# Performance work log

Measured on AMD Instinct MI355X. Metric: run time of the kernel, lower is better.

Reference implementation:

```python
import jax, jax.numpy as jnp
import numpy as np

D_MODEL = 1024
N_HEAD = 16
HEAD_SIZE = D_MODEL // N_HEAD


def setup_inputs() -> dict:
    key = jax.random.key(0)
    ks = jax.random.split(key, 7)
    B, T, E = 2, 2048, D_MODEL
    scale = 0.02
    return {
        "q": jax.random.normal(ks[0], (B, T, E), dtype=jnp.float32),
        "k": jax.random.normal(ks[1], (B, T, E), dtype=jnp.float32),
        "v": jax.random.normal(ks[2], (B, T, E), dtype=jnp.float32),
        "Wq": jax.random.normal(ks[3], (E, E), dtype=jnp.float32) * scale,
        "Wk": jax.random.normal(ks[4], (E, E), dtype=jnp.float32) * scale,
        "Wv": jax.random.normal(ks[5], (E, E), dtype=jnp.float32) * scale,
        "Wo": jax.random.normal(ks[6], (E, E), dtype=jnp.float32) * scale,
    }


def reference(q, k, v, Wq, Wk, Wv, Wo):
    B, T, E = q.shape
    # torch nn.Linear(bias=False): y = x @ W.T
    qh = (q @ Wq.T).reshape(B, T, N_HEAD, HEAD_SIZE).transpose(0, 2, 1, 3)  # [B,H,T,Dh]
    kh = (k @ Wk.T).reshape(B, T, N_HEAD, HEAD_SIZE).transpose(0, 2, 1, 3)
    vh = (v @ Wv.T).reshape(B, T, N_HEAD, HEAD_SIZE).transpose(0, 2, 1, 3)

    scale = 1.0 / jnp.sqrt(jnp.asarray(HEAD_SIZE, dtype=q.dtype))
    wei = jnp.einsum("bhqd,bhkd->bhqk", qh, kh) * scale  # [B,H,T,T]

    # causal mask (tril): positions j > i set to -inf
    causal = jnp.tril(jnp.ones((T, T), dtype=bool))
    wei = jnp.where(causal, wei, jnp.asarray(-jnp.inf, dtype=wei.dtype))

    attn = jax.nn.softmax(wei, axis=-1)
    out = jnp.einsum("bhqk,bhkd->bhqd", attn, vh)  # [B,H,T,Dh]
    out = out.transpose(0, 2, 1, 3).reshape(B, T, E)
    return out @ Wo.T  # dropout p=0.0 -> identity
```

## Files before the change

kernel.cpp:

```cpp
#include <hip/hip_runtime.h>
#include <hip/hip_bf16.h>
#include <cstddef>
#include <cstdint>

#define B_SZ   2
#define T_SEQ  2048
#define E_DIM  1024
#define N_HEAD 16
#define HEAD   64

typedef unsigned short u16;
typedef unsigned int u32;
using frag8 = __attribute__((ext_vector_type(8))) short;
using f32x4 = __attribute__((ext_vector_type(4))) float;

__device__ inline u16 f2bf(float x) {
    __hip_bfloat16 h = __float2bfloat16(x);
    return *reinterpret_cast<u16*>(&h);
}

__device__ inline void gl2lds16(const void* g, void* l) {
    auto gp = reinterpret_cast<const __attribute__((address_space(1))) unsigned int*>(
        reinterpret_cast<uintptr_t>(g));
    auto lp = reinterpret_cast<__attribute__((address_space(3))) unsigned int*>(
        reinterpret_cast<uintptr_t>(l));
    __builtin_amdgcn_global_load_lds(gp, lp, 16, 0, 0);
}

struct CastArgs {
    const float* src[7];
    u16* dst[7];
    int n[7];
    float scale[7];
};

__global__ __launch_bounds__(256) void cast_f32_bf16(CastArgs a) {
    const int t = blockIdx.y;
    const int i0 = (blockIdx.x * 256 + threadIdx.x) * 8;
    if (i0 >= a.n[t]) return;
    const float sc = a.scale[t];
    const float4 f0 = *(const float4*)(a.src[t] + i0);
    const float4 f1 = *(const float4*)(a.src[t] + i0 + 4);
    union { u16 s[8]; uint4 v; } r;
    r.s[0] = f2bf(f0.x * sc); r.s[1] = f2bf(f0.y * sc);
    r.s[2] = f2bf(f0.z * sc); r.s[3] = f2bf(f0.w * sc);
    r.s[4] = f2bf(f1.x * sc); r.s[5] = f2bf(f1.y * sc);
    r.s[6] = f2bf(f1.z * sc); r.s[7] = f2bf(f1.w * sc);
    *(uint4*)(a.dst[t] + i0) = r.v;
}

__device__ inline void gemm_core(const u16* __restrict__ X,
                                 const u16* __restrict__ W,
                                 void* __restrict__ Yv, int mode,
                                 int bm0, int bn0) {
    __shared__ u16 As[2][128 * 64];
    __shared__ u16 Bs[2][128 * 64];

    const int tid = threadIdx.x;
    const int w = tid >> 6;
    const int lane = tid & 63;
    const int ln = lane & 15;
    const int quad = lane >> 4;
    const int wm = (w & 1) * 64;
    const int wn = (w >> 1) * 64;

    const int l8 = lane >> 3;
    const int g = (lane & 7) ^ l8;

    const u16* Ag = X + (size_t)(bm0 + w * 32 + l8) * 1024 + g * 8;
    const u16* Bg = W + (size_t)(bn0 + w * 32 + l8) * 1024 + g * 8;
    const int al = __builtin_amdgcn_readfirstlane(w * 2048);
    const int bl = __builtin_amdgcn_readfirstlane(w * 2048);

    const f32x4 zf = {0.f, 0.f, 0.f, 0.f};
    f32x4 acc[4][4];
#pragma unroll
    for (int mi = 0; mi < 4; ++mi)
#pragma unroll
        for (int nj = 0; nj < 4; ++nj) acc[mi][nj] = zf;

    const int sw = ln & 7;

#pragma unroll
    for (int it = 0; it < 4; ++it) {
        gl2lds16(Ag + (size_t)it * 8 * 1024, &As[0][0] + al + it * 512);
        gl2lds16(Bg + (size_t)it * 8 * 1024, &Bs[0][0] + bl + it * 512);
    }

    for (int k0 = 0; k0 < 1024; k0 += 64) {
        const int buf = (k0 >> 6) & 1;
        __syncthreads();

        if (k0 + 64 < 1024) {
#pragma unroll
            for (int it = 0; it < 4; ++it) {
                gl2lds16(Ag + (size_t)it * 8 * 1024 + k0 + 64,
                         &As[buf ^ 1][0] + al + it * 512);
                gl2lds16(Bg + (size_t)it * 8 * 1024 + k0 + 64,
                         &Bs[buf ^ 1][0] + bl + it * 512);
            }
        }

        frag8 a[4][2], b[4][2];
#pragma unroll
        for (int kc = 0; kc < 2; ++kc) {
            const int slot = ((kc * 4 + quad) ^ sw) * 8;
#pragma unroll
            for (int mi = 0; mi < 4; ++mi)
                a[mi][kc] = *(const frag8*)(&As[buf][0] + (wm + mi * 16 + ln) * 64 + slot);
#pragma unroll
            for (int nj = 0; nj < 4; ++nj)
                b[nj][kc] = *(const frag8*)(&Bs[buf][0] + (wn + nj * 16 + ln) * 64 + slot);
        }
#pragma unroll
        for (int kc = 0; kc < 2; ++kc)
#pragma unroll
            for (int mi = 0; mi < 4; ++mi)
#pragma unroll
                for (int nj = 0; nj < 4; ++nj)
                    acc[mi][nj] = __builtin_amdgcn_mfma_f32_16x16x32_bf16(
                        a[mi][kc], b[nj][kc], acc[mi][nj], 0, 0, 0);
    }

#pragma unroll
    for (int mi = 0; mi < 4; ++mi)
#pragma unroll
        for (int nj = 0; nj < 4; ++nj)
#pragma unroll
            for (int reg = 0; reg < 4; ++reg) {
                const int m = bm0 + wm + mi * 16 + quad * 4 + reg;
                const int n = bn0 + wn + nj * 16 + ln;
                if (mode == 1) {
                    ((float*)Yv)[(size_t)m * E_DIM + n] = acc[mi][nj][reg];
                } else {
                    const int b_ = m >> 11, t_ = m & (T_SEQ - 1);
                    const int h_ = n >> 6, d_ = n & (HEAD - 1);
                    const size_t idx = (mode == 0)
                        ? (((size_t)(b_ * N_HEAD + h_)) * T_SEQ + t_) * HEAD + d_
                        : (((size_t)(b_ * N_HEAD + h_)) * HEAD + d_) * T_SEQ + t_;
                    ((u16*)Yv)[idx] = f2bf(acc[mi][nj][reg]);
                }
            }
}

struct QkvArgs {
    const u16* X[3];
    const u16* W[3];
    u16* Y[3];
};

__global__ __launch_bounds__(256, 2) void gemm_qkv(QkvArgs a) {
    const int z = blockIdx.z;
    gemm_core(a.X[z], a.W[z], a.Y[z], z == 2 ? 2 : 0,
              blockIdx.x * 128, blockIdx.y * 128);
}

__global__ __launch_bounds__(256, 2) void gemm_out(const u16* __restrict__ X,
                                                   const u16* __restrict__ W,
                                                   float* __restrict__ Y) {
    gemm_core(X, W, Y, 1, blockIdx.x * 128, blockIdx.y * 128);
}

__global__ __launch_bounds__(512, 4) void attn_mfma(const u16* __restrict__ Qh,
                                                    const u16* __restrict__ Kh,
                                                    const u16* __restrict__ Vt_g,
                                                    u16* __restrict__ Aa) {
    __shared__ u16 Ks[2][128 * 64];
    __shared__ u16 Vs[2][64 * 128];

    const int tid = threadIdx.x;
    const int w = tid >> 6;
    const int wq = w & 3;
    const int wk = w >> 2;
    const int lane = tid & 63;
    const int ln = lane & 15;
    const int quad = lane >> 4;

    const int i = blockIdx.x;
    const int half = i >> 8;
    const int r_ = i & 255;
    const int bh = r_ >> 3;
    const int j = r_ & 7;
    const int qt = half ? j : (15 - j);
    const int q0 = qt * 128;
    const int qw = q0 + wq * 32;

    const size_t base = (size_t)bh * T_SEQ * HEAD;
    const u16* Qb = Qh + base;
    const u16* Kb = Kh + base;
    const u16* Vtb = Vt_g + base;

    const int l8 = lane >> 3;
    const int gk = (lane & 7) ^ l8;
    const int l16 = lane >> 4;
    const int c16 = lane & 15;
    const int sls = __builtin_amdgcn_readfirstlane(w * 1024);

    frag8 qf[2][2];
#pragma unroll
    for (int qq = 0; qq < 2; ++qq)
#pragma unroll
        for (int kc = 0; kc < 2; ++kc)
            qf[qq][kc] = *(const frag8*)(Qb + (size_t)(qw + qq * 16 + ln) * HEAD +
                                         kc * 32 + quad * 8);

    const f32x4 zf = {0.f, 0.f, 0.f, 0.f};
    f32x4 o[4][2];
    float rsl[2] = {0.f, 0.f};
#pragma unroll
    for (int dt = 0; dt < 4; ++dt)
#pragma unroll
        for (int qq = 0; qq < 2; ++qq) o[dt][qq] = zf;

    const int ktiles = qt + 1;

#pragma unroll
    for (int it = 0; it < 2; ++it) {
        const int krow = w * 16 + it * 8 + l8;
        gl2lds16(Kb + (size_t)krow * HEAD + gk * 8, &Ks[0][0] + sls + it * 512);
        const int vrow = w * 8 + it * 4 + l16;
        const int gv = c16 ^ (vrow & 7);
        gl2lds16(Vtb + (size_t)vrow * T_SEQ + gv * 8, &Vs[0][0] + sls + it * 512);
    }

    const int sw = ln & 7;
    const int hsel = quad >> 1;
    const int s_lo = ((quad & 1) * 2) * 16 + ln;
    const int s_hi = s_lo + 16;

    for (int kt = 0; kt < ktiles; ++kt) {
        const int k0 = kt << 7;
        const int buf = kt & 1;
        __syncthreads();

        if (kt + 1 < ktiles) {
            const int k1 = k0 + 128;
#pragma unroll
            for (int it = 0; it < 2; ++it) {
                const int krow = w * 16 + it * 8 + l8;
                gl2lds16(Kb + (size_t)(k1 + krow) * HEAD + gk * 8,
                         &Ks[buf ^ 1][0] + sls + it * 512);
                const int vrow = w * 8 + it * 4 + l16;
                const int gv = c16 ^ (vrow & 7);
                gl2lds16(Vtb + (size_t)vrow * T_SEQ + k1 + gv * 8,
                         &Vs[buf ^ 1][0] + sls + it * 512);
            }
        }

        const int kbase = k0 + wk * 64;
        if (kbase <= qw + 31) {
            const bool msk = (kbase + 63 > qw);
            u32 pk[4][2][2];
#pragma unroll
            for (int kk = 0; kk < 4; ++kk) {
                f32x4 st[2] = {zf, zf};
#pragma unroll
                for (int kc = 0; kc < 2; ++kc) {
                    const int slot = ((kc * 4 + quad) ^ sw) * 8;
                    const frag8 kf = *(const frag8*)(&Ks[buf][0] +
                                                     (wk * 64 + kk * 16 + ln) * 64 + slot);
                    st[0] = __builtin_amdgcn_mfma_f32_16x16x32_bf16(kf, qf[0][kc], st[0], 0, 0, 0);
                    st[1] = __builtin_amdgcn_mfma_f32_16x16x32_bf16(kf, qf[1][kc], st[1], 0, 0, 0);
                }
#pragma unroll
                for (int qq = 0; qq < 2; ++qq) {
                    float e[4];
#pragma unroll
                    for (int reg = 0; reg < 4; ++reg) {
                        const int key = kbase + kk * 16 + quad * 4 + reg;
                        const int qg = qw + qq * 16 + ln;
                        float ev = __expf(st[qq][reg]);
                        if (msk) ev = (key <= qg) ? ev : 0.f;
                        e[reg] = ev;
                        rsl[qq] += ev;
                    }
                    pk[kk][qq][0] = ((u32)f2bf(e[1]) << 16) | f2bf(e[0]);
                    pk[kk][qq][1] = ((u32)f2bf(e[3]) << 16) | f2bf(e[2]);
                }
            }

#pragma unroll
            for (int kc = 0; kc < 2; ++kc) {
                union { frag8 f; u32 d[4]; } pb[2];
#pragma unroll
                for (int qq = 0; qq < 2; ++qq) {
                    const u32 a00 = __shfl(pk[kc * 2][qq][0], s_lo, 64);
                    const u32 a01 = __shfl(pk[kc * 2][qq][1], s_lo, 64);
                    const u32 a02 = __shfl(pk[kc * 2][qq][0], s_hi, 64);
                    const u32 a03 = __shfl(pk[kc * 2][qq][1], s_hi, 64);
                    const u32 a10 = __shfl(pk[kc * 2 + 1][qq][0], s_lo, 64);
                    const u32 a11 = __shfl(pk[kc * 2 + 1][qq][1], s_lo, 64);
                    const u32 a12 = __shfl(pk[kc * 2 + 1][qq][0], s_hi, 64);
                    const u32 a13 = __shfl(pk[kc * 2 + 1][qq][1], s_hi, 64);
                    pb[qq].d[0] = hsel ? a10 : a00;
                    pb[qq].d[1] = hsel ? a11 : a01;
                    pb[qq].d[2] = hsel ? a12 : a02;
                    pb[qq].d[3] = hsel ? a13 : a03;
                }
                const int slotv = (((wk * 2 + kc) * 4 + quad) ^ sw) * 8;
#pragma unroll
                for (int dt = 0; dt < 4; ++dt) {
                    const frag8 vf = *(const frag8*)(&Vs[buf][0] + (dt * 16 + ln) * 128 + slotv);
                    o[dt][0] = __builtin_amdgcn_mfma_f32_16x16x32_bf16(vf, pb[0].f, o[dt][0], 0, 0, 0);
                    o[dt][1] = __builtin_amdgcn_mfma_f32_16x16x32_bf16(vf, pb[1].f, o[dt][1], 0, 0, 0);
                }
            }
        }
    }

#pragma unroll
    for (int qq = 0; qq < 2; ++qq) {
        rsl[qq] += __shfl_xor(rsl[qq], 16, 64);
        rsl[qq] += __shfl_xor(rsl[qq], 32, 64);
    }

    __syncthreads();
    float* ored = (float*)&Ks[0][0];
    float* lred = (float*)&Vs[0][0];
    if (wk == 1) {
#pragma unroll
        for (int dt = 0; dt < 4; ++dt)
#pragma unroll
            for (int qq = 0; qq < 2; ++qq)
#pragma unroll
                for (int rg = 0; rg < 4; ++rg)
                    ored[(dt * 8 + qq * 4 + rg) * 256 + wq * 64 + lane] = o[dt][qq][rg];
        lred[wq * 64 + lane] = rsl[0];
        lred[256 + wq * 64 + lane] = rsl[1];
    }
    __syncthreads();
    if (wk == 0) {
#pragma unroll
        for (int dt = 0; dt < 4; ++dt)
#pragma unroll
            for (int qq = 0; qq < 2; ++qq)
#pragma unroll
                for (int rg = 0; rg < 4; ++rg)
                    o[dt][qq][rg] += ored[(dt * 8 + qq * 4 + rg) * 256 + wq * 64 + lane];
        rsl[0] += lred[wq * 64 + lane];
        rsl[1] += lred[256 + wq * 64 + lane];

        const float inv0 = 1.f / rsl[0];
        const float inv1 = 1.f / rsl[1];
        const int b_ = bh >> 4, h_ = bh & (N_HEAD - 1);
#pragma unroll
        for (int qq = 0; qq < 2; ++qq) {
            const float inv = qq ? inv1 : inv0;
            const int qg = qw + qq * 16 + ln;
            u16* rowp = Aa + ((size_t)(b_ * T_SEQ + qg)) * E_DIM + h_ * HEAD;
#pragma unroll
            for (int dt = 0; dt < 4; ++dt)
#pragma unroll
                for (int rp = 0; rp < 2; ++rp) {
                    const u32 v = ((u32)f2bf(o[dt][qq][2 * rp + 1] * inv) << 16) |
                                  f2bf(o[dt][qq][2 * rp] * inv);
                    *(u32*)(rowp + dt * 16 + quad * 4 + rp * 2) = v;
                }
        }
    }
}

extern "C" void kernel_launch(void* const* d_in, const int* in_sizes, int n_in,
                              void* d_out, int out_size, void* d_ws, size_t ws_size,
                              hipStream_t stream) {
    const float* q  = (const float*)d_in[0];
    const float* k  = (const float*)d_in[1];
    const float* v  = (const float*)d_in[2];
    const float* Wq = (const float*)d_in[3];
    const float* Wk = (const float*)d_in[4];
    const float* Wv = (const float*)d_in[5];
    const float* Wo = (const float*)d_in[6];

    u16* ws = (u16*)d_ws;
    const size_t M4 = (size_t)4 * 1024 * 1024;
    const size_t M1 = (size_t)1024 * 1024;
    u16* qb  = ws;
    u16* kb  = ws + M4;
    u16* vb  = ws + 2 * M4;
    u16* Wqb = ws + 3 * M4;
    u16* Wkb = ws + 3 * M4 + M1;
    u16* Wvb = ws + 3 * M4 + 2 * M1;
    u16* Wob = ws + 3 * M4 + 3 * M1;
    u16* Qh  = ws + 4 * M4;
    u16* Kh  = ws + 5 * M4;
    u16* Vht = ws + 6 * M4;
    u16* Aa  = ws + 7 * M4;

    CastArgs ca;
    ca.src[0] = q;  ca.src[1] = k;  ca.src[2] = v;
    ca.src[3] = Wq; ca.src[4] = Wk; ca.src[5] = Wv; ca.src[6] = Wo;
    ca.dst[0] = qb;  ca.dst[1] = kb;  ca.dst[2] = vb;
    ca.dst[3] = Wqb; ca.dst[4] = Wkb; ca.dst[5] = Wvb; ca.dst[6] = Wob;
    ca.n[0] = ca.n[1] = ca.n[2] = (int)M4;
    ca.n[3] = ca.n[4] = ca.n[5] = ca.n[6] = (int)M1;
    ca.scale[0] = ca.scale[1] = ca.scale[2] = 1.f;
    ca.scale[3] = 0.125f;
    ca.scale[4] = ca.scale[5] = ca.scale[6] = 1.f;
    cast_f32_bf16<<<dim3(2048, 7), 256, 0, stream>>>(ca);

    QkvArgs ga;
    ga.X[0] = qb;  ga.X[1] = kb;  ga.X[2] = vb;
    ga.W[0] = Wqb; ga.W[1] = Wkb; ga.W[2] = Wvb;
    ga.Y[0] = Qh;  ga.Y[1] = Kh;  ga.Y[2] = Vht;
    gemm_qkv<<<dim3(32, 8, 3), 256, 0, stream>>>(ga);

    attn_mfma<<<dim3(512), 512, 0, stream>>>(Qh, Kh, Vht, Aa);

    gemm_out<<<dim3(32, 8), 256, 0, stream>>>(Aa, Wob, (float*)d_out);
}
```

Before: 196.3 us.

## Triple-buffer GEMM K-loop with 32-wide slices and fine-grained waitcnt

Restructures the shared GEMM core from a double-buffered 64-wide K step into a triple-buffered 32-wide K step, with a prefetch distance of two stages. It replaces __syncthreads with explicit vmcnt waits and raw barriers, adds s_setprio around the MFMA block, and uses a new XOR swizzle for the 32-column tiles. Occupancy hints rise to 3 blocks per CU. The aim is to hide global-to-LDS latency better and raise occupancy, at the cost of more barriers per unit of K work and reliance on hand-counted vmcnt values.

After: 208.3 us. +6.1%, slower.

```diff
diff --git a/kernel.cpp b/kernel.cpp
--- a/kernel.cpp
+++ b/kernel.cpp
@@ -53,8 +53,8 @@
                                  const u16* __restrict__ W,
                                  void* __restrict__ Yv, int mode,
                                  int bm0, int bn0) {
-    __shared__ u16 As[2][128 * 64];
-    __shared__ u16 Bs[2][128 * 64];
+    __shared__ u16 As[3][128 * 32];
+    __shared__ u16 Bs[3][128 * 32];
 
     const int tid = threadIdx.x;
     const int w = tid >> 6;
@@ -64,13 +64,10 @@
     const int wm = (w & 1) * 64;
     const int wn = (w >> 1) * 64;
 
-    const int l8 = lane >> 3;
-    const int g = (lane & 7) ^ l8;
-
-    const u16* Ag = X + (size_t)(bm0 + w * 32 + l8) * 1024 + g * 8;
-    const u16* Bg = W + (size_t)(bn0 + w * 32 + l8) * 1024 + g * 8;
-    const int al = __builtin_amdgcn_readfirstlane(w * 2048);
-    const int bl = __builtin_amdgcn_readfirstlane(w * 2048);
+    const int r4 = lane >> 2;
+    const int gch = (lane & 3) ^ (r4 & 3);
+    const int sdst = __builtin_amdgcn_readfirstlane(w * 1024);
+    const int xk = (quad ^ (ln & 3)) * 8;
 
     const f32x4 zf = {0.f, 0.f, 0.f, 0.f};
     f32x4 acc[4][4];
@@ -79,47 +76,52 @@
 #pragma unroll
         for (int nj = 0; nj < 4; ++nj) acc[mi][nj] = zf;
 
-    const int sw = ln & 7;
-
-#pragma unroll
-    for (int it = 0; it < 4; ++it) {
-        gl2lds16(Ag + (size_t)it * 8 * 1024, &As[0][0] + al + it * 512);
-        gl2lds16(Bg + (size_t)it * 8 * 1024, &Bs[0][0] + bl + it * 512);
-    }
-
-    for (int k0 = 0; k0 < 1024; k0 += 64) {
-        const int buf = (k0 >> 6) & 1;
-        __syncthreads();
-
-        if (k0 + 64 < 1024) {
-#pragma unroll
-            for (int it = 0; it < 4; ++it) {
-                gl2lds16(Ag + (size_t)it * 8 * 1024 + k0 + 64,
-                         &As[buf ^ 1][0] + al + it * 512);
-                gl2lds16(Bg + (size_t)it * 8 * 1024 + k0 + 64,
-                         &Bs[buf ^ 1][0] + bl + it * 512);
-            }
+    auto stage = [&](int hh, int slot) {
+        const int col = hh * 32 + gch * 8;
+#pragma unroll
+        for (int i = 0; i < 2; ++i) {
+            gl2lds16(X + (size_t)(bm0 + w * 32 + i * 16 + r4) * 1024 + col,
+                     &As[slot][0] + sdst + i * 512);
+            gl2lds16(W + (size_t)(bn0 + w * 32 + i * 16 + r4) * 1024 + col,
+                     &Bs[slot][0] + sdst + i * 512);
         }
-
-        frag8 a[4][2], b[4][2];
-#pragma unroll
-        for (int kc = 0; kc < 2; ++kc) {
-            const int slot = ((kc * 4 + quad) ^ sw) * 8;
-#pragma unroll
-            for (int mi = 0; mi < 4; ++mi)
-                a[mi][kc] = *(const frag8*)(&As[buf][0] + (wm + mi * 16 + ln) * 64 + slot);
+    };
+
+    stage(0, 0);
+    stage(1, 1);
+    asm volatile("s_waitcnt vmcnt(4)" ::: "memory");
+    __builtin_amdgcn_s_barrier();
+    asm volatile("" ::: "memory");
+
+#pragma unroll
+    for (int h = 0; h < 32; ++h) {
+        const int slot = h % 3;
+
+        frag8 a[4], b[4];
+#pragma unroll
+        for (int mi = 0; mi < 4; ++mi)
+            a[mi] = *(const frag8*)(&As[slot][0] + (wm + mi * 16 + ln) * 32 + xk);
+#pragma unroll
+        for (int nj = 0; nj < 4; ++nj)
+            b[nj] = *(const frag8*)(&Bs[slot][0] + (wn + nj * 16 + ln) * 32 + xk);
+
+        if (h + 2 < 32) stage(h + 2, (h + 2) % 3);
+
+        if (h <= 29)      asm volatile("s_waitcnt vmcnt(4)" ::: "memory");
+        else if (h == 30) asm volatile("s_waitcnt vmcnt(0)" ::: "memory");
+
+        __builtin_amdgcn_s_setprio(1);
+#pragma unroll
+        for (int mi = 0; mi < 4; ++mi)
 #pragma unroll
             for (int nj = 0; nj < 4; ++nj)
-                b[nj][kc] = *(const frag8*)(&Bs[buf][0] + (wn + nj * 16 + ln) * 64 + slot);
-        }
-#pragma unroll
-        for (int kc = 0; kc < 2; ++kc)
-#pragma unroll
-            for (int mi = 0; mi < 4; ++mi)
-#pragma unroll
-                for (int nj = 0; nj < 4; ++nj)
-                    acc[mi][nj] = __builtin_amdgcn_mfma_f32_16x16x32_bf16(
-                        a[mi][kc], b[nj][kc], acc[mi][nj], 0, 0, 0);
+                acc[mi][nj] = __builtin_amdgcn_mfma_f32_16x16x32_bf16(
+                    a[mi], b[nj], acc[mi][nj], 0, 0, 0);
+        __builtin_amdgcn_s_setprio(0);
+
+        asm volatile("" ::: "memory");
+        __builtin_amdgcn_s_barrier();
+        asm volatile("" ::: "memory");
     }
 
 #pragma unroll
@@ -149,13 +151,13 @@
     u16* Y[3];
 };
 
-__global__ __launch_bounds__(256, 2) void gemm_qkv(QkvArgs a) {
+__global__ __launch_bounds__(256, 3) void gemm_qkv(QkvArgs a) {
     const int z = blockIdx.z;
     gemm_core(a.X[z], a.W[z], a.Y[z], z == 2 ? 2 : 0,
               blockIdx.x * 128, blockIdx.y * 128);
 }
 
-__global__ __launch_bounds__(256, 2) void gemm_out(const u16* __restrict__ X,
+__global__ __launch_bounds__(256, 3) void gemm_out(const u16* __restrict__ X,
                                                    const u16* __restrict__ W,
                                                    float* __restrict__ Y) {
     gemm_core(X, W, Y, 1, blockIdx.x * 128, blockIdx.y * 128);
```
